# Kernel tuning notes

Hardware: AMD Instinct MI355X
Metric: run time of the kernel (lower is better)

Reference implementation:

```python
import jax, jax.numpy as jnp
import numpy as np

B, N, C = 8, 1024, 640   # frames, tokens per frame (32x32), channels
H, D = 8, 80             # heads, dim per head; inner = H*D = 640
R = 3                    # adaptive context_range (uniform, odd)
SCALE = D ** -0.5


def _window_indices(batch_size, context_range):
    """Replicates the per-sample index construction in RefAttention.forward.
    First half of the batch attends within [0, B//2-1], second within [B//2, B-1]."""
    half = batch_size // 2
    hr = (context_range - 1) // 2
    rows = []
    for i in range(batch_size):
        lo_b, hi_b = (0, half - 1) if i < half else (half, batch_size - 1)
        ci = list(range(max(lo_b, i - hr), min(hi_b, i + hr + 1)))  # arange(a, min(hi_b, i+hr+1))
        while len(ci) < context_range:
            if ci[0] > lo_b:
                ci = [ci[0] - 1] + ci
            if len(ci) < context_range and ci[-1] < hi_b:
                ci = ci + [ci[-1] + 1]
        rows.append(ci)
    return np.asarray(rows, dtype=np.int32)  # [B, R]


def setup_inputs() -> dict:
    key = jax.random.key(0)
    ks = jax.random.split(key, 6)
    inner = H * D
    x = jax.random.normal(ks[0], (B, N, C), dtype=jnp.float32)
    s = 1.0 / np.sqrt(C)
    Wq = jax.random.normal(ks[1], (inner, C), dtype=jnp.float32) * s
    Wk = jax.random.normal(ks[2], (inner, C), dtype=jnp.float32) * s
    Wv = jax.random.normal(ks[3], (inner, C), dtype=jnp.float32) * s
    Wo = jax.random.normal(ks[4], (C, inner), dtype=jnp.float32) * (1.0 / np.sqrt(inner))
    bo = jnp.zeros((C,), dtype=jnp.float32)
    ctx_idx = jnp.asarray(_window_indices(B, R))  # [B, R] int32, static window gather indices
    return {"x": x, "Wq": Wq, "Wk": Wk, "Wv": Wv, "Wo": Wo, "bo": bo, "ctx_idx": ctx_idx}


def reference(x, Wq, Wk, Wv, Wo, bo, ctx_idx):
    # projections (nn.Linear, no bias): y = x @ W^T
    q = jnp.einsum('bnc,ic->bni', x, Wq)                      # [B, N, inner]
    k = jnp.einsum('bnc,ic->bni', x, Wk)                      # context defaults to x
    v = jnp.einsum('bnc,ic->bni', x, Wv)
    # original uses k.data / v.data (detached); forward value is identical
    qh = q.reshape(B, N, H, D)
    # gather per-frame K/V windows: [B, R, N, inner] -> [B, R*N, H, D]
    kw = k[ctx_idx].reshape(B, R * N, H, D)
    vw = v[ctx_idx].reshape(B, R * N, H, D)
    sim = jnp.einsum('bnhd,bmhd->bhnm', qh, kw) * SCALE       # [B, H, N, R*N]
    attn = jax.nn.softmax(sim, axis=-1)
    out = jnp.einsum('bhnm,bmhd->bnhd', attn, vw).reshape(B, N, H * D)
    return jnp.einsum('bni,ci->bnc', out, Wo) + bo            # to_out (dropout p=0)
```

## Files before the change

kernel.cpp:

```cpp
#include <hip/hip_runtime.h>
#include <hip/hip_bf16.h>

#define BB    8
#define NNTOK 1024
#define CCH   640
#define HH    8
#define DHD   80
#define RRW   3
#define MM    (BB * NNTOK)
#define INNER 640
#define SCALE 0.111803398874989484820458954f
#define QSCALE (SCALE * 1.44269504088896340736f)

#define KSTR 88
#define VSTR 72

typedef __bf16 bf16x8 __attribute__((ext_vector_type(8)));
typedef float  f32x4  __attribute__((ext_vector_type(4)));

__device__ __forceinline__ unsigned short f2b(float f) {
    union { float f; unsigned int u; } v; v.f = f;
    unsigned int r = v.u + 0x7fffu + ((v.u >> 16) & 1u);
    return (unsigned short)(r >> 16);
}
__device__ __forceinline__ bf16x8 zero8() {
    bf16x8 z;
#pragma unroll
    for (int i = 0; i < 8; i++) z[i] = (__bf16)0.0f;
    return z;
}
__device__ __forceinline__ f32x4 zero4() {
    f32x4 z;
#pragma unroll
    for (int i = 0; i < 4; i++) z[i] = 0.0f;
    return z;
}
__device__ __forceinline__ float fexp2(float x) {
#if __has_builtin(__builtin_amdgcn_exp2f)
    return __builtin_amdgcn_exp2f(x);
#else
    return __expf(x * 0.69314718055994530942f);
#endif
}

__global__ __launch_bounds__(256) void castk(const float* __restrict__ s,
                                             unsigned short* __restrict__ d, int n) {
    int i = (blockIdx.x * 256 + threadIdx.x) * 4;
    if (i < n) {
        float4 f = *(const float4*)(s + i);
        ushort4 o;
        o.x = f2b(f.x); o.y = f2b(f.y); o.z = f2b(f.z); o.w = f2b(f.w);
        *(ushort4*)(d + i) = o;
    }
}

__global__ __launch_bounds__(256) void castw4(
    const float* __restrict__ w0, const float* __restrict__ w1,
    const float* __restrict__ w2, const float* __restrict__ w3,
    unsigned short* __restrict__ d0, unsigned short* __restrict__ d1,
    unsigned short* __restrict__ d2, unsigned short* __restrict__ d3, int n)
{
    const float* s; unsigned short* d;
    switch (blockIdx.y) {
        case 0: s = w0; d = d0; break;
        case 1: s = w1; d = d1; break;
        case 2: s = w2; d = d2; break;
        default: s = w3; d = d3; break;
    }
    int i = (blockIdx.x * 256 + threadIdx.x) * 4;
    if (i < n) {
        float4 f = *(const float4*)(s + i);
        ushort4 o;
        o.x = f2b(f.x); o.y = f2b(f.y); o.z = f2b(f.z); o.w = f2b(f.w);
        *(ushort4*)(d + i) = o;
    }
}

__global__ __launch_bounds__(256) void proj_qkv_mfma(
    const unsigned short* __restrict__ xb,
    const unsigned short* __restrict__ wqb,
    const unsigned short* __restrict__ wkb,
    const unsigned short* __restrict__ wvb,
    unsigned short* __restrict__ q16, unsigned short* __restrict__ k16,
    unsigned short* __restrict__ vto)
{
    __shared__ __align__(16) unsigned short Xs[64 * 72];
    __shared__ __align__(16) unsigned short Wsh[64 * 72];
    const int t = threadIdx.x;
    const int wvid = t >> 6, lane = t & 63, col = lane & 15, quad = lane >> 4;
    const int m0 = blockIdx.x * 64, i0 = blockIdx.y * 64, z = blockIdx.z;
    const unsigned short* W = (z == 0) ? wqb : (z == 1) ? wkb : wvb;
    const int row = t >> 2, seg = t & 3;

    f32x4 acc[4];
#pragma unroll
    for (int nt = 0; nt < 4; nt++) acc[nt] = zero4();

    for (int kt = 0; kt < INNER; kt += 64) {
        uint4 x0 = *(const uint4*)(xb + (size_t)(m0 + row) * INNER + kt + seg * 16);
        uint4 x1 = *(const uint4*)(xb + (size_t)(m0 + row) * INNER + kt + seg * 16 + 8);
        uint4 w0 = *(const uint4*)(W  + (size_t)(i0 + row) * INNER + kt + seg * 16);
        uint4 w1 = *(const uint4*)(W  + (size_t)(i0 + row) * INNER + kt + seg * 16 + 8);
        __syncthreads();
        *(uint4*)&Xs[row * 72 + seg * 16]      = x0;
        *(uint4*)&Xs[row * 72 + seg * 16 + 8]  = x1;
        *(uint4*)&Wsh[row * 72 + seg * 16]     = w0;
        *(uint4*)&Wsh[row * 72 + seg * 16 + 8] = w1;
        __syncthreads();
#pragma unroll
        for (int kbk = 0; kbk < 2; kbk++) {
            bf16x8 af = *(const bf16x8*)&Xs[(wvid * 16 + col) * 72 + kbk * 32 + quad * 8];
#pragma unroll
            for (int nt = 0; nt < 4; nt++) {
                bf16x8 bfr = *(const bf16x8*)&Wsh[(nt * 16 + col) * 72 + kbk * 32 + quad * 8];
                acc[nt] = __builtin_amdgcn_mfma_f32_16x16x32_bf16(af, bfr, acc[nt], 0, 0, 0);
            }
        }
    }
    if (z == 0) {
#pragma unroll
        for (int nt = 0; nt < 4; nt++)
#pragma unroll
            for (int r = 0; r < 4; r++)
                q16[(size_t)(m0 + wvid * 16 + quad * 4 + r) * INNER + i0 + nt * 16 + col] = f2b(acc[nt][r] * QSCALE);
    } else if (z == 1) {
#pragma unroll
        for (int nt = 0; nt < 4; nt++)
#pragma unroll
            for (int r = 0; r < 4; r++)
                k16[(size_t)(m0 + wvid * 16 + quad * 4 + r) * INNER + i0 + nt * 16 + col] = f2b(acc[nt][r]);
    } else {
#pragma unroll
        for (int nt = 0; nt < 4; nt++) {
            int i = i0 + nt * 16 + col;
            int h = i / DHD, dd = i % DHD;
#pragma unroll
            for (int r = 0; r < 4; r++) {
                int m = m0 + wvid * 16 + quad * 4 + r;
                int bfm = m >> 10, n = m & (NNTOK - 1);
                vto[((size_t)(bfm * HH + h) * DHD + dd) * NNTOK + n] = f2b(acc[nt][r]);
            }
        }
    }
}

__device__ __forceinline__ int ksrow(int tau) {
    return (((tau >> 5) * 2 + ((tau >> 2) & 1)) << 4) + (((tau >> 3) & 3) << 2) + (tau & 3);
}

__global__ __launch_bounds__(512, 4) void attn_mfma9(
    const unsigned short* __restrict__ qb, const unsigned short* __restrict__ kb,
    const unsigned short* __restrict__ vt, const int* __restrict__ ctx,
    unsigned short* __restrict__ ao)
{
    __shared__ __align__(16) unsigned short Ks[2][64 * KSTR];
    __shared__ __align__(16) unsigned short Vt[2][DHD * VSTR];
    const int t = threadIdx.x;
    const int wvid = t >> 6, lane = t & 63, col = lane & 15, quad = lane >> 4;
    const int qt = blockIdx.x, h = blockIdx.y, b = blockIdx.z;

    bf16x8 qf0, qf1, qf2;
    {
        const unsigned short* qp = qb + (size_t)(b * NNTOK + qt * 128 + wvid * 16 + col) * INNER + h * DHD;
        qf0 = *(const bf16x8*)(qp + quad * 8);
        qf1 = *(const bf16x8*)(qp + 32 + quad * 8);
        qf2 = zero8();
        if (quad < 2) qf2 = *(const bf16x8*)(qp + 64 + quad * 8);
    }
    f32x4 o[5];
#pragma unroll
    for (int dt = 0; dt < 5; dt++) o[dt] = zero4();
    float lp = 0.0f;

    const int ki0 = t, ki1 = t + 512;
    const int ktok0 = ki0 / 10, kseg0 = ki0 % 10;
    const int ktok1 = ki1 / 10, kseg1 = ki1 % 10;
    const int ksr0 = ksrow(ktok0), ksr1 = ksrow(ktok1);
    const int vd0 = ki0 >> 3, vs0 = ki0 & 7;
    const int vd1 = ki1 >> 3, vs1 = ki1 & 7;

    {
        const int fr = ctx[b * RRW];
        const unsigned short* kbase = kb + (size_t)(fr * NNTOK) * INNER + h * DHD;
        const unsigned short* vbase = vt + ((size_t)(fr * HH + h) * DHD) * NNTOK;
        uint4 ka0 = *(const uint4*)(kbase + (size_t)ktok0 * INNER + kseg0 * 8);
        uint4 va0 = *(const uint4*)(vbase + (size_t)vd0 * NNTOK + vs0 * 8);
        *(uint4*)&Ks[0][ksr0 * KSTR + kseg0 * 8] = ka0;
        *(uint4*)&Vt[0][vd0 * VSTR + vs0 * 8] = va0;
        if (t < 128) {
            uint4 ka1 = *(const uint4*)(kbase + (size_t)ktok1 * INNER + kseg1 * 8);
            uint4 va1 = *(const uint4*)(vbase + (size_t)vd1 * NNTOK + vs1 * 8);
            *(uint4*)&Ks[0][ksr1 * KSTR + kseg1 * 8] = ka1;
            *(uint4*)&Vt[0][vd1 * VSTR + vs1 * 8] = va1;
        }
    }

    for (int kc = 0; kc < (RRW * NNTOK) / 64; kc++) {
        __syncthreads();

        const int kcn = (kc + 1 < 48) ? kc + 1 : 47;
        const int frn = ctx[b * RRW + (kcn >> 4)];
        const int tokn = (kcn & 15) * 64;
        const unsigned short* kbase = kb + (size_t)(frn * NNTOK + tokn) * INNER + h * DHD;
        const unsigned short* vbase = vt + ((size_t)(frn * HH + h) * DHD) * NNTOK + tokn;
        uint4 ka0 = *(const uint4*)(kbase + (size_t)ktok0 * INNER + kseg0 * 8);
        uint4 va0 = *(const uint4*)(vbase + (size_t)vd0 * NNTOK + vs0 * 8);
        uint4 ka1, va1;
        if (t < 128) {
            ka1 = *(const uint4*)(kbase + (size_t)ktok1 * INNER + kseg1 * 8);
            va1 = *(const uint4*)(vbase + (size_t)vd1 * NNTOK + vs1 * 8);
        }

        const unsigned short* ksr = &Ks[kc & 1][0];
        const unsigned short* vtr = &Vt[kc & 1][0];

        f32x4 s[4];
#pragma unroll
        for (int n0 = 0; n0 < 4; n0++) {
            const unsigned short* kp = ksr + (n0 * 16 + col) * KSTR;
            bf16x8 k0 = *(const bf16x8*)(kp + quad * 8);
            bf16x8 k1 = *(const bf16x8*)(kp + 32 + quad * 8);
            bf16x8 k2 = zero8();
            if (quad < 2) k2 = *(const bf16x8*)(kp + 64 + quad * 8);
            f32x4 sv = zero4();
            sv = __builtin_amdgcn_mfma_f32_16x16x32_bf16(k0, qf0, sv, 0, 0, 0);
            sv = __builtin_amdgcn_mfma_f32_16x16x32_bf16(k1, qf1, sv, 0, 0, 0);
            sv = __builtin_amdgcn_mfma_f32_16x16x32_bf16(k2, qf2, sv, 0, 0, 0);
            s[n0] = sv;
        }
        bf16x8 pa0, pa1;
        float l0 = 0.0f, l1 = 0.0f;
#pragma unroll
        for (int n0 = 0; n0 < 4; n0++) {
            float p0 = fexp2(s[n0][0]), p1 = fexp2(s[n0][1]);
            float p2 = fexp2(s[n0][2]), p3 = fexp2(s[n0][3]);
            if (n0 < 2) l0 += (p0 + p1) + (p2 + p3);
            else        l1 += (p0 + p1) + (p2 + p3);
            const int j0 = (n0 & 1) * 4;
            if (n0 < 2) {
                pa0[j0]     = (__bf16)p0; pa0[j0 + 1] = (__bf16)p1;
                pa0[j0 + 2] = (__bf16)p2; pa0[j0 + 3] = (__bf16)p3;
            } else {
                pa1[j0]     = (__bf16)p0; pa1[j0 + 1] = (__bf16)p1;
                pa1[j0 + 2] = (__bf16)p2; pa1[j0 + 3] = (__bf16)p3;
            }
        }
        lp += l0 + l1;
#pragma unroll
        for (int dt = 0; dt < 5; dt++) {
            const unsigned short* vp = vtr + (dt * 16 + col) * VSTR;
            bf16x8 v0 = *(const bf16x8*)(vp + quad * 8);
            bf16x8 v1 = *(const bf16x8*)(vp + 32 + quad * 8);
            o[dt] = __builtin_amdgcn_mfma_f32_16x16x32_bf16(pa0, v0, o[dt], 0, 0, 0);
            o[dt] = __builtin_amdgcn_mfma_f32_16x16x32_bf16(pa1, v1, o[dt], 0, 0, 0);
        }
        {
            unsigned short* ksb = &Ks[(kc + 1) & 1][0];
            unsigned short* vtb = &Vt[(kc + 1) & 1][0];
            *(uint4*)&ksb[ksr0 * KSTR + kseg0 * 8] = ka0;
            *(uint4*)&vtb[vd0 * VSTR + vs0 * 8] = va0;
            if (t < 128) {
                *(uint4*)&ksb[ksr1 * KSTR + kseg1 * 8] = ka1;
                *(uint4*)&vtb[vd1 * VSTR + vs1 * 8] = va1;
            }
        }
    }
    float lsum = lp;
    lsum += __shfl_xor(lsum, 16);
    lsum += __shfl_xor(lsum, 32);
    float inv[4];
#pragma unroll
    for (int r = 0; r < 4; r++)
        inv[r] = 1.0f / __shfl(lsum, quad * 4 + r);
#pragma unroll
    for (int r = 0; r < 4; r++) {
        unsigned short* op = ao + (size_t)(b * NNTOK + qt * 128 + wvid * 16 + quad * 4 + r) * INNER + h * DHD;
#pragma unroll
        for (int dt = 0; dt < 5; dt++)
            op[dt * 16 + col] = f2b(o[dt][r] * inv[r]);
    }
}

__global__ __launch_bounds__(256) void proj_out_mfma(
    const unsigned short* __restrict__ ab, const unsigned short* __restrict__ wob,
    const float* __restrict__ bo, float* __restrict__ out)
{
    __shared__ __align__(16) unsigned short Xs[64 * 72];
    __shared__ __align__(16) unsigned short Wsh[64 * 72];
    const int t = threadIdx.x;
    const int wvid = t >> 6, lane = t & 63, col = lane & 15, quad = lane >> 4;
    const int m0 = blockIdx.x * 64, i0 = blockIdx.y * 64;
    const int row = t >> 2, seg = t & 3;

    float bias[4];
#pragma unroll
    for (int nt = 0; nt < 4; nt++) bias[nt] = bo[i0 + nt * 16 + col];

    f32x4 acc[4];
#pragma unroll
    for (int nt = 0; nt < 4; nt++) acc[nt] = zero4();

    for (int kt = 0; kt < INNER; kt += 64) {
        uint4 x0 = *(const uint4*)(ab  + (size_t)(m0 + row) * INNER + kt + seg * 16);
        uint4 x1 = *(const uint4*)(ab  + (size_t)(m0 + row) * INNER + kt + seg * 16 + 8);
        uint4 w0 = *(const uint4*)(wob + (size_t)(i0 + row) * INNER + kt + seg * 16);
        uint4 w1 = *(const uint4*)(wob + (size_t)(i0 + row) * INNER + kt + seg * 16 + 8);
        __syncthreads();
        *(uint4*)&Xs[row * 72 + seg * 16]      = x0;
        *(uint4*)&Xs[row * 72 + seg * 16 + 8]  = x1;
        *(uint4*)&Wsh[row * 72 + seg * 16]     = w0;
        *(uint4*)&Wsh[row * 72 + seg * 16 + 8] = w1;
        __syncthreads();
#pragma unroll
        for (int kbk = 0; kbk < 2; kbk++) {
            bf16x8 af = *(const bf16x8*)&Xs[(wvid * 16 + col) * 72 + kbk * 32 + quad * 8];
#pragma unroll
            for (int nt = 0; nt < 4; nt++) {
                bf16x8 bfr = *(const bf16x8*)&Wsh[(nt * 16 + col) * 72 + kbk * 32 + quad * 8];
                acc[nt] = __builtin_amdgcn_mfma_f32_16x16x32_bf16(af, bfr, acc[nt], 0, 0, 0);
            }
        }
    }
#pragma unroll
    for (int nt = 0; nt < 4; nt++)
#pragma unroll
        for (int r = 0; r < 4; r++)
            out[(size_t)(m0 + wvid * 16 + quad * 4 + r) * CCH + i0 + nt * 16 + col] = acc[nt][r] + bias[nt];
}

extern "C" void kernel_launch(void* const* d_in, const int* in_sizes, int n_in,
                              void* d_out, int out_size, void* d_ws, size_t ws_size,
                              hipStream_t stream) {
    const float* x  = (const float*)d_in[0];
    const float* wq = (const float*)d_in[1];
    const float* wk = (const float*)d_in[2];
    const float* wv = (const float*)d_in[3];
    const float* wo = (const float*)d_in[4];
    const float* bo = (const float*)d_in[5];
    const int* ctx  = (const int*)d_in[6];
    float* out = (float*)d_out;

    const size_t XN = (size_t)MM * INNER;
    const size_t WN = (size_t)INNER * CCH;
    unsigned short* q16 = (unsigned short*)d_ws;
    unsigned short* k16 = q16 + XN;
    unsigned short* vto = k16 + XN;
    unsigned short* xb  = vto + XN;
    unsigned short* aob = xb;
    unsigned short* wqb = xb + XN;
    unsigned short* wkb = wqb + WN;
    unsigned short* wvb = wkb + WN;
    unsigned short* wob = wvb + WN;

    castk<<<dim3((XN / 4 + 255) / 256), 256, 0, stream>>>(x, xb, (int)XN);
    castw4<<<dim3((WN / 4 + 255) / 256, 4), 256, 0, stream>>>(wq, wk, wv, wo, wqb, wkb, wvb, wob, (int)WN);

    proj_qkv_mfma<<<dim3(MM / 64, INNER / 64, 3), 256, 0, stream>>>(xb, wqb, wkb, wvb, q16, k16, vto);
    attn_mfma9<<<dim3(NNTOK / 128, HH, BB), 512, 0, stream>>>(q16, k16, vto, ctx, aob);
    proj_out_mfma<<<dim3(MM / 64, CCH / 64), 256, 0, stream>>>(aob, wob, bo, out);
}
```

Measured before the change: 224.3 us.

## Process two query row tiles per wave to reuse K/V LDS fragments

The attention kernel moves from 8 waves per block to 4 waves, and each wave now handles 32 query rows as two 16-row tiles instead of 16. Each K and V fragment read from LDS feeds two MFMAs, which halves LDS read traffic per unit of compute and interleaves independent MFMA chains. Each thread now stages more K/V loads per chunk. The cost is higher register pressure (double accumulators, scores and Q fragments) and fewer waves per block, which may reduce latency hiding.

```diff
diff --git a/kernel.cpp b/kernel.cpp
--- a/kernel.cpp
+++ b/kernel.cpp
@@ -148,7 +148,7 @@
     return (((tau >> 5) * 2 + ((tau >> 2) & 1)) << 4) + (((tau >> 3) & 3) << 2) + (tau & 3);
 }
 
-__global__ __launch_bounds__(512, 4) void attn_mfma9(
+__global__ __launch_bounds__(256, 2) void attn_mfma10(
     const unsigned short* __restrict__ qb, const unsigned short* __restrict__ kb,
     const unsigned short* __restrict__ vt, const int* __restrict__ ctx,
     unsigned short* __restrict__ ao)
@@ -159,39 +159,50 @@
     const int wvid = t >> 6, lane = t & 63, col = lane & 15, quad = lane >> 4;
     const int qt = blockIdx.x, h = blockIdx.y, b = blockIdx.z;
 
-    bf16x8 qf0, qf1, qf2;
+    bf16x8 qfA0, qfA1, qfA2, qfB0, qfB1, qfB2;
     {
-        const unsigned short* qp = qb + (size_t)(b * NNTOK + qt * 128 + wvid * 16 + col) * INNER + h * DHD;
-        qf0 = *(const bf16x8*)(qp + quad * 8);
-        qf1 = *(const bf16x8*)(qp + 32 + quad * 8);
-        qf2 = zero8();
-        if (quad < 2) qf2 = *(const bf16x8*)(qp + 64 + quad * 8);
-    }
-    f32x4 o[5];
-#pragma unroll
-    for (int dt = 0; dt < 5; dt++) o[dt] = zero4();
-    float lp = 0.0f;
-
-    const int ki0 = t, ki1 = t + 512;
-    const int ktok0 = ki0 / 10, kseg0 = ki0 % 10;
-    const int ktok1 = ki1 / 10, kseg1 = ki1 % 10;
-    const int ksr0 = ksrow(ktok0), ksr1 = ksrow(ktok1);
-    const int vd0 = ki0 >> 3, vs0 = ki0 & 7;
-    const int vd1 = ki1 >> 3, vs1 = ki1 & 7;
+        const unsigned short* qpA = qb + (size_t)(b * NNTOK + qt * 128 + wvid * 32 + col) * INNER + h * DHD;
+        const unsigned short* qpB = qpA + (size_t)16 * INNER;
+        qfA0 = *(const bf16x8*)(qpA + quad * 8);
+        qfA1 = *(const bf16x8*)(qpA + 32 + quad * 8);
+        qfB0 = *(const bf16x8*)(qpB + quad * 8);
+        qfB1 = *(const bf16x8*)(qpB + 32 + quad * 8);
+        qfA2 = zero8(); qfB2 = zero8();
+        if (quad < 2) {
+            qfA2 = *(const bf16x8*)(qpA + 64 + quad * 8);
+            qfB2 = *(const bf16x8*)(qpB + 64 + quad * 8);
+        }
+    }
+    f32x4 oA[5], oB[5];
+#pragma unroll
+    for (int dt = 0; dt < 5; dt++) { oA[dt] = zero4(); oB[dt] = zero4(); }
+    float lpA = 0.0f, lpB = 0.0f;
+
+    const int i0 = t, i1 = t + 256, i2 = t + 512;
+    const int ktok0 = i0 / 10, kseg0 = i0 % 10, ksr0 = ksrow(ktok0);
+    const int ktok1 = i1 / 10, kseg1 = i1 % 10, ksr1 = ksrow(ktok1);
+    const int ktok2 = i2 / 10, kseg2 = i2 % 10, ksr2 = ksrow(ktok2);
+    const int vd0 = i0 >> 3, vs0 = i0 & 7;
+    const int vd1 = i1 >> 3, vs1 = i1 & 7;
+    const int vd2 = i2 >> 3, vs2 = i2 & 7;
 
     {
         const int fr = ctx[b * RRW];
         const unsigned short* kbase = kb + (size_t)(fr * NNTOK) * INNER + h * DHD;
         const unsigned short* vbase = vt + ((size_t)(fr * HH + h) * DHD) * NNTOK;
         uint4 ka0 = *(const uint4*)(kbase + (size_t)ktok0 * INNER + kseg0 * 8);
+        uint4 ka1 = *(const uint4*)(kbase + (size_t)ktok1 * INNER + kseg1 * 8);
         uint4 va0 = *(const uint4*)(vbase + (size_t)vd0 * NNTOK + vs0 * 8);
+        uint4 va1 = *(const uint4*)(vbase + (size_t)vd1 * NNTOK + vs1 * 8);
         *(uint4*)&Ks[0][ksr0 * KSTR + kseg0 * 8] = ka0;
+        *(uint4*)&Ks[0][ksr1 * KSTR + kseg1 * 8] = ka1;
         *(uint4*)&Vt[0][vd0 * VSTR + vs0 * 8] = va0;
+        *(uint4*)&Vt[0][vd1 * VSTR + vs1 * 8] = va1;
         if (t < 128) {
-            uint4 ka1 = *(const uint4*)(kbase + (size_t)ktok1 * INNER + kseg1 * 8);
-            uint4 va1 = *(const uint4*)(vbase + (size_t)vd1 * NNTOK + vs1 * 8);
-            *(uint4*)&Ks[0][ksr1 * KSTR + kseg1 * 8] = ka1;
-            *(uint4*)&Vt[0][vd1 * VSTR + vs1 * 8] = va1;
+            uint4 ka2 = *(const uint4*)(kbase + (size_t)ktok2 * INNER + kseg2 * 8);
+            uint4 va2 = *(const uint4*)(vbase + (size_t)vd2 * NNTOK + vs2 * 8);
+            *(uint4*)&Ks[0][ksr2 * KSTR + kseg2 * 8] = ka2;
+            *(uint4*)&Vt[0][vd2 * VSTR + vs2 * 8] = va2;
         }
     }
 
@@ -204,17 +215,19 @@
         const unsigned short* kbase = kb + (size_t)(frn * NNTOK + tokn) * INNER + h * DHD;
         const unsigned short* vbase = vt + ((size_t)(frn * HH + h) * DHD) * NNTOK + tokn;
         uint4 ka0 = *(const uint4*)(kbase + (size_t)ktok0 * INNER + kseg0 * 8);
+        uint4 ka1 = *(const uint4*)(kbase + (size_t)ktok1 * INNER + kseg1 * 8);
         uint4 va0 = *(const uint4*)(vbase + (size_t)vd0 * NNTOK + vs0 * 8);
-        uint4 ka1, va1;
+        uint4 va1 = *(const uint4*)(vbase + (size_t)vd1 * NNTOK + vs1 * 8);
+        uint4 ka2, va2;
         if (t < 128) {
-            ka1 = *(const uint4*)(kbase + (size_t)ktok1 * INNER + kseg1 * 8);
-            va1 = *(const uint4*)(vbase + (size_t)vd1 * NNTOK + vs1 * 8);
+            ka2 = *(const uint4*)(kbase + (size_t)ktok2 * INNER + kseg2 * 8);
+            va2 = *(const uint4*)(vbase + (size_t)vd2 * NNTOK + vs2 * 8);
         }
 
         const unsigned short* ksr = &Ks[kc & 1][0];
         const unsigned short* vtr = &Vt[kc & 1][0];
 
-        f32x4 s[4];
+        f32x4 sA[4], sB[4];
 #pragma unroll
         for (int n0 = 0; n0 < 4; n0++) {
             const unsigned short* kp = ksr + (n0 * 16 + col) * KSTR;
@@ -222,62 +235,74 @@
             bf16x8 k1 = *(const bf16x8*)(kp + 32 + quad * 8);
             bf16x8 k2 = zero8();
             if (quad < 2) k2 = *(const bf16x8*)(kp + 64 + quad * 8);
-            f32x4 sv = zero4();
-            sv = __builtin_amdgcn_mfma_f32_16x16x32_bf16(k0, qf0, sv, 0, 0, 0);
-            sv = __builtin_amdgcn_mfma_f32_16x16x32_bf16(k1, qf1, sv, 0, 0, 0);
-            sv = __builtin_amdgcn_mfma_f32_16x16x32_bf16(k2, qf2, sv, 0, 0, 0);
-            s[n0] = sv;
-        }
-        bf16x8 pa0, pa1;
-        float l0 = 0.0f, l1 = 0.0f;
+            f32x4 svA = zero4(), svB = zero4();
+            svA = __builtin_amdgcn_mfma_f32_16x16x32_bf16(k0, qfA0, svA, 0, 0, 0);
+            svB = __builtin_amdgcn_mfma_f32_16x16x32_bf16(k0, qfB0, svB, 0, 0, 0);
+            svA = __builtin_amdgcn_mfma_f32_16x16x32_bf16(k1, qfA1, svA, 0, 0, 0);
+            svB = __builtin_amdgcn_mfma_f32_16x16x32_bf16(k1, qfB1, svB, 0, 0, 0);
+            svA = __builtin_amdgcn_mfma_f32_16x16x32_bf16(k2, qfA2, svA, 0, 0, 0);
+            svB = __builtin_amdgcn_mfma_f32_16x16x32_bf16(k2, qfB2, svB, 0, 0, 0);
+            sA[n0] = svA; sB[n0] = svB;
+        }
+        bf16x8 paA0, paA1, paB0, paB1;
 #pragma unroll
         for (int n0 = 0; n0 < 4; n0++) {
-            float p0 = fexp2(s[n0][0]), p1 = fexp2(s[n0][1]);
-            float p2 = fexp2(s[n0][2]), p3 = fexp2(s[n0][3]);
-            if (n0 < 2) l0 += (p0 + p1) + (p2 + p3);
-            else        l1 += (p0 + p1) + (p2 + p3);
             const int j0 = (n0 & 1) * 4;
+            float a0 = fexp2(sA[n0][0]), a1 = fexp2(sA[n0][1]);
+            float a2 = fexp2(sA[n0][2]), a3 = fexp2(sA[n0][3]);
+            lpA += (a0 + a1) + (a2 + a3);
+            float b0 = fexp2(sB[n0][0]), b1 = fexp2(sB[n0][1]);
+            float b2 = fexp2(sB[n0][2]), b3 = fexp2(sB[n0][3]);
+            lpB += (b0 + b1) + (b2 + b3);
             if (n0 < 2) {
-                pa0[j0]     = (__bf16)p0; pa0[j0 + 1] = (__bf16)p1;
-                pa0[j0 + 2] = (__bf16)p2; pa0[j0 + 3] = (__bf16)p3;
+                paA0[j0] = (__bf16)a0; paA0[j0+1] = (__bf16)a1; paA0[j0+2] = (__bf16)a2; paA0[j0+3] = (__bf16)a3;
+                paB0[j0] = (__bf16)b0; paB0[j0+1] = (__bf16)b1; paB0[j0+2] = (__bf16)b2; paB0[j0+3] = (__bf16)b3;
             } else {
-                pa1[j0]     = (__bf16)p0; pa1[j0 + 1] = (__bf16)p1;
-                pa1[j0 + 2] = (__bf16)p2; pa1[j0 + 3] = (__bf16)p3;
-            }
-        }
-        lp += l0 + l1;
+                paA1[j0] = (__bf16)a0; paA1[j0+1] = (__bf16)a1; paA1[j0+2] = (__bf16)a2; paA1[j0+3] = (__bf16)a3;
+                paB1[j0] = (__bf16)b0; paB1[j0+1] = (__bf16)b1; paB1[j0+2] = (__bf16)b2; paB1[j0+3] = (__bf16)b3;
+            }
+        }
 #pragma unroll
         for (int dt = 0; dt < 5; dt++) {
             const unsigned short* vp = vtr + (dt * 16 + col) * VSTR;
             bf16x8 v0 = *(const bf16x8*)(vp + quad * 8);
             bf16x8 v1 = *(const bf16x8*)(vp + 32 + quad * 8);
-            o[dt] = __builtin_amdgcn_mfma_f32_16x16x32_bf16(pa0, v0, o[dt], 0, 0, 0);
-            o[dt] = __builtin_amdgcn_mfma_f32_16x16x32_bf16(pa1, v1, o[dt], 0, 0, 0);
+            oA[dt] = __builtin_amdgcn_mfma_f32_16x16x32_bf16(paA0, v0, oA[dt], 0, 0, 0);
+            oB[dt] = __builtin_amdgcn_mfma_f32_16x16x32_bf16(paB0, v0, oB[dt], 0, 0, 0);
+            oA[dt] = __builtin_amdgcn_mfma_f32_16x16x32_bf16(paA1, v1, oA[dt], 0, 0, 0);
+            oB[dt] = __builtin_amdgcn_mfma_f32_16x16x32_bf16(paB1, v1, oB[dt], 0, 0, 0);
         }
         {
             unsigned short* ksb = &Ks[(kc + 1) & 1][0];
             unsigned short* vtb = &Vt[(kc + 1) & 1][0];
             *(uint4*)&ksb[ksr0 * KSTR + kseg0 * 8] = ka0;
+            *(uint4*)&ksb[ksr1 * KSTR + kseg1 * 8] = ka1;
             *(uint4*)&vtb[vd0 * VSTR + vs0 * 8] = va0;
+            *(uint4*)&vtb[vd1 * VSTR + vs1 * 8] = va1;
             if (t < 128) {
-                *(uint4*)&ksb[ksr1 * KSTR + kseg1 * 8] = ka1;
-                *(uint4*)&vtb[vd1 * VSTR + vs1 * 8] = va1;
-            }
-        }
-    }
-    float lsum = lp;
-    lsum += __shfl_xor(lsum, 16);
-    lsum += __shfl_xor(lsum, 32);
-    float inv[4];
-#pragma unroll
-    for (int r = 0; r < 4; r++)
-        inv[r] = 1.0f / __shfl(lsum, quad * 4 + r);
+                *(uint4*)&ksb[ksr2 * KSTR + kseg2 * 8] = ka2;
+                *(uint4*)&vtb[vd2 * VSTR + vs2 * 8] = va2;
+            }
+        }
+    }
+    float lsA = lpA, lsB = lpB;
+    lsA += __shfl_xor(lsA, 16); lsA += __shfl_xor(lsA, 32);
+    lsB += __shfl_xor(lsB, 16); lsB += __shfl_xor(lsB, 32);
+    float invA[4], invB[4];
 #pragma unroll
     for (int r = 0; r < 4; r++) {
-        unsigned short* op = ao + (size_t)(b * NNTOK + qt * 128 + wvid * 16 + quad * 4 + r) * INNER + h * DHD;
-#pragma unroll
-        for (int dt = 0; dt < 5; dt++)
-            op[dt * 16 + col] = f2b(o[dt][r] * inv[r]);
+        invA[r] = 1.0f / __shfl(lsA, quad * 4 + r);
+        invB[r] = 1.0f / __shfl(lsB, quad * 4 + r);
+    }
+#pragma unroll
+    for (int r = 0; r < 4; r++) {
+        unsigned short* opA = ao + (size_t)(b * NNTOK + qt * 128 + wvid * 32 + quad * 4 + r) * INNER + h * DHD;
+        unsigned short* opB = opA + (size_t)16 * INNER;
+#pragma unroll
+        for (int dt = 0; dt < 5; dt++) {
+            opA[dt * 16 + col] = f2b(oA[dt][r] * invA[r]);
+            opB[dt * 16 + col] = f2b(oB[dt][r] * invB[r]);
+        }
     }
 }
 
@@ -356,6 +381,6 @@
     castw4<<<dim3((WN / 4 + 255) / 256, 4), 256, 0, stream>>>(wq, wk, wv, wo, wqb, wkb, wvb, wob, (int)WN);
 
     proj_qkv_mfma<<<dim3(MM / 64, INNER / 64, 3), 256, 0, stream>>>(xb, wqb, wkb, wvb, q16, k16, vto);
-    attn_mfma9<<<dim3(NNTOK / 128, HH, BB), 512, 0, stream>>>(q16, k16, vto, ctx, aob);
+    attn_mfma10<<<dim3(NNTOK / 128, HH, BB), 256, 0, stream>>>(q16, k16, vto, ctx, aob);
     proj_out_mfma<<<dim3(MM / 64, CCH / 64), 256, 0, stream>>>(aob, wob, bo, out);
 }
```

Result: faster. 217.7 us (-2.9%).
